# Performance work log

Measured on AMD Instinct MI355X. Metric: run time of the kernel, lower is better.

The kernel has to match this reference:

```python
import jax, jax.numpy as jnp
import numpy as np

B, S, H = 2, 2048, 1024
NH = 16
HD = H // NH  # 64


def setup_inputs() -> dict:
    key = jax.random.key(0)
    ks = jax.random.split(key, 12)
    s = 1.0 / np.sqrt(H)
    return {
        "x_q": jax.random.normal(ks[0], (B, S, H), jnp.float32),
        "x_k": jax.random.normal(ks[1], (B, S, H), jnp.float32),
        "x_v": jax.random.normal(ks[2], (B, S, H), jnp.float32),
        "attention_mask": jax.random.randint(ks[3], (B, S), 0, 2, jnp.int32),
        "Wq": jax.random.normal(ks[4], (H, H), jnp.float32) * s,
        "bq": jnp.zeros((H,), jnp.float32),
        "Wk": jax.random.normal(ks[5], (H, H), jnp.float32) * s,
        "bk": jnp.zeros((H,), jnp.float32),
        "Wv": jax.random.normal(ks[6], (H, H), jnp.float32) * s,
        "bv": jnp.zeros((H,), jnp.float32),
        "Wo": jax.random.normal(ks[7], (H, H), jnp.float32) * s,
        "bo": jnp.zeros((H,), jnp.float32),
    }


def reference(x_q, x_k, x_v, attention_mask, Wq, bq, Wk, bk, Wv, bv, Wo, bo):
    b, s, h = x_q.shape
    # projections
    q = x_q @ Wq + bq
    k = x_k @ Wk + bk
    v = x_v @ Wv + bv
    # [B, NH, S, HD]
    q = q.reshape(b, s, NH, HD).transpose(0, 2, 1, 3)
    k = k.reshape(b, s, NH, HD).transpose(0, 2, 1, 3)
    v = v.reshape(b, s, NH, HD).transpose(0, 2, 1, 3)
    scores = jnp.einsum("bhqd,bhkd->bhqk", q, k) / jnp.sqrt(jnp.float32(HD))
    # key-padding mask: 1 -> keep (0 bias), else -inf; broadcast [B,1,1,S]
    bias = jnp.where(attention_mask == 1, 0.0, -jnp.inf).astype(scores.dtype)
    scores = scores + bias[:, None, None, :]
    attn = jax.nn.softmax(scores, axis=-1)
    # dropout prob = 0.0 (eval / deterministic): identity
    out = jnp.einsum("bhqk,bhkd->bhqd", attn, v)
    out = out.transpose(0, 2, 1, 3).reshape(b, s, h)
    return out @ Wo + bo
```

## Files before the change

kernel.cpp:

```cpp
#include <hip/hip_runtime.h>

#define DEVI static __device__ __forceinline__

typedef unsigned short u16;
typedef unsigned int u32;
typedef __attribute__((ext_vector_type(8))) __bf16 bf16x8;
typedef __attribute__((ext_vector_type(8))) short short8;
typedef __attribute__((ext_vector_type(4))) float f32x4;
typedef __attribute__((ext_vector_type(16))) float f32x16;
typedef __attribute__((ext_vector_type(4))) u32 u32x4;

DEVI u16 f2bf(float f) {
  union { float f; u32 u; } v; v.f = f;
  u32 r = v.u + 0x7fffu + ((v.u >> 16) & 1u);
  return (u16)(r >> 16);
}

DEVI u16 bfc(float f) {
  union { __bf16 b; u16 u; } v; v.b = (__bf16)f; return v.u;
}

DEVI void gload16(const void* g, void* l) {
  __builtin_amdgcn_global_load_lds(
      (const __attribute__((address_space(1))) void*)g,
      (__attribute__((address_space(3))) void*)l,
      16, 0, 0);
}

__global__ void k_cvt(const float* __restrict__ in, u16* __restrict__ out, int n4) {
  int i = blockIdx.x * blockDim.x + threadIdx.x;
  if (i >= n4) return;
  const float4 v = reinterpret_cast<const float4*>(in)[i];
  ushort4 o;
  o.x = f2bf(v.x); o.y = f2bf(v.y); o.z = f2bf(v.z); o.w = f2bf(v.w);
  reinterpret_cast<ushort4*>(out)[i] = o;
}

__global__ void k_maskbias(const int* __restrict__ m, float* __restrict__ bias, int n) {
  int i = blockIdx.x * blockDim.x + threadIdx.x;
  if (i < n) bias[i] = (m[i] == 1) ? 0.f : -1e30f;
}

__global__ void k_transcvt(const float* __restrict__ W, u16* __restrict__ Wt) {
  __shared__ float tl[32][33];
  const int n0 = blockIdx.x * 32, k0 = blockIdx.y * 32;
  const int tx = threadIdx.x, ty = threadIdx.y;
#pragma unroll
  for (int r = ty; r < 32; r += 8)
    tl[r][tx] = W[(size_t)(k0 + r) * 1024 + n0 + tx];
  __syncthreads();
#pragma unroll
  for (int r = ty; r < 32; r += 8)
    Wt[(size_t)(n0 + r) * 1024 + k0 + tx] = f2bf(tl[tx][r]);
}

DEVI void store1(u16* C, size_t i, float v) { C[i] = f2bf(v); }
DEVI void store1(float* C, size_t i, float v) { C[i] = v; }

template <typename OutT>
__global__ __launch_bounds__(256, 2) void k_gemm_bt(
    const u16* __restrict__ Abase, long aZ,
    const u16* __restrict__ Btbase, long bZ,
    const float* __restrict__ bias0, const float* __restrict__ bias1,
    const float* __restrict__ bias2,
    float s0, float s1, float s2,
    OutT* __restrict__ Cbase, long cZ, u16* __restrict__ Vt,
    int M, int N, int K) {
  const int z = blockIdx.z;
  const u16* A  = Abase  + (size_t)z * aZ;
  const u16* Bt = Btbase + (size_t)z * bZ;
  OutT* C = Cbase + (size_t)z * cZ;
  const float* bias = (z == 0) ? bias0 : ((z == 1) ? bias1 : bias2);
  const float scl = (z == 0) ? s0 : ((z == 1) ? s1 : s2);

  __shared__ u16 lsA[128 * 32];
  __shared__ u16 lsB[128 * 32];

  const int t = threadIdx.x;
  const int w = t >> 6, ln = t & 63;
  const int l15 = ln & 15, lhi = ln >> 4;
  const int wr = w >> 1, wc = w & 1;
  const int m0 = blockIdx.x * 128, n0 = blockIdx.y * 128;

  f32x4 acc[4][4] = {};

  for (int kt = 0; kt < K; kt += 32) {
#pragma unroll
    for (int i = 0; i < 2; ++i) {
      const int li = i * 256 + t;
      const int row = li >> 2, cb = (li & 3) << 3;
      gload16(A + (size_t)(m0 + row) * K + kt + cb,
              (char*)lsA + (i * 256 + w * 64) * 16);
      gload16(Bt + (size_t)(n0 + row) * K + kt + cb,
              (char*)lsB + (i * 256 + w * 64) * 16);
    }
    __syncthreads();

    bf16x8 af[4], bf_[4];
#pragma unroll
    for (int m = 0; m < 4; ++m)
      af[m] = *reinterpret_cast<const bf16x8*>(
          &lsA[(wr * 64 + m * 16 + l15) * 32 + lhi * 8]);
#pragma unroll
    for (int n = 0; n < 4; ++n)
      bf_[n] = *reinterpret_cast<const bf16x8*>(
          &lsB[(wc * 64 + n * 16 + l15) * 32 + lhi * 8]);
#pragma unroll
    for (int m = 0; m < 4; ++m)
#pragma unroll
      for (int n = 0; n < 4; ++n)
        acc[m][n] = __builtin_amdgcn_mfma_f32_16x16x32_bf16(af[m], bf_[n], acc[m][n], 0, 0, 0);
    __syncthreads();
  }

  if (Vt != nullptr && z == 2) {
#pragma unroll
    for (int n = 0; n < 4; ++n) {
      const int c = n0 + wc * 64 + n * 16 + l15;
      const float bv = bias[c];
#pragma unroll
      for (int m = 0; m < 4; ++m) {
        const int r = m0 + wr * 64 + m * 16 + lhi * 4;
        ushort4 s4;
#pragma unroll
        for (int j = 0; j < 4; ++j) ((u16*)&s4)[j] = f2bf(acc[m][n][j] + bv);
        *reinterpret_cast<ushort4*>(
            &Vt[((size_t)((r >> 11) * 1024 + c)) * 2048 + (r & 2047)]) = s4;
      }
    }
    return;
  }

#pragma unroll
  for (int n = 0; n < 4; ++n) {
    const int c = n0 + wc * 64 + n * 16 + l15;
    const float bv = bias[c];
#pragma unroll
    for (int m = 0; m < 4; ++m)
#pragma unroll
      for (int j = 0; j < 4; ++j) {
        const int r = m0 + wr * 64 + m * 16 + lhi * 4 + j;
        store1(C, (size_t)r * N + c, (acc[m][n][j] + bv) * scl);
      }
  }
}

__global__ __launch_bounds__(256, 2) void k_attn(
    const u16* __restrict__ Q, const u16* __restrict__ K, const u16* __restrict__ Vt,
    const float* __restrict__ MB, u16* __restrict__ O) {
  __shared__ u16 lsK[2][64][72];
  __shared__ u16 lsV[2][64][72];

  const int t = threadIdx.x, w = t >> 6, ln = t & 63;
  const int l31 = ln & 31, h = ln >> 5, h8 = h * 8;
  const int fid = blockIdx.x;
  const int xcd = fid & 7, slot = fid >> 3;
  const int pair = xcd * 4 + (slot >> 4);
  const int qt = slot & 15;
  const int hh = pair & 15, b = pair >> 4;

  const size_t rowQ = (size_t)b * 2048 + qt * 128 + w * 32;
  const int hc = hh * 64;

  const int srow = t >> 3, scol = (t & 7) << 3;
  const u16* Kg = K + ((size_t)b * 2048 + srow) * 1024 + hc + scol;
  const int half = t & 1;
  const int g16 = ((t & 7) >> 1) << 4;
  const u16* VgA = Vt + ((size_t)(b * 1024 + hc) + srow) * 2048 + g16 + 4 * half;
  const float* MBb = MB + b * 2048;

  bf16x8 qb[4];
#pragma unroll
  for (int ks = 0; ks < 4; ++ks)
    qb[ks] = *reinterpret_cast<const bf16x8*>(
        &Q[(rowQ + l31) * 1024 + hc + ks * 16 + h8]);

  f32x16 o[2] = {};
  float mrow = -1e30f, lsum = 0.f;

  short8 rk0, rk1;
  ushort4 rv0a, rv0b, rv1a, rv1b;
  rk0 = *reinterpret_cast<const short8*>(Kg);
  rk1 = *reinterpret_cast<const short8*>(Kg + 32 * 1024);
  rv0a = *reinterpret_cast<const ushort4*>(VgA);
  rv0b = *reinterpret_cast<const ushort4*>(VgA + 8);
  rv1a = *reinterpret_cast<const ushort4*>(VgA + 32 * 2048);
  rv1b = *reinterpret_cast<const ushort4*>(VgA + 32 * 2048 + 8);
  *reinterpret_cast<short8*>(&lsK[0][srow][scol]) = rk0;
  *reinterpret_cast<short8*>(&lsK[0][32 + srow][scol]) = rk1;
  *reinterpret_cast<ushort4*>(&lsV[0][srow][scol]) = rv0a;
  *reinterpret_cast<ushort4*>(&lsV[0][srow][scol + 4]) = rv0b;
  *reinterpret_cast<ushort4*>(&lsV[0][32 + srow][scol]) = rv1a;
  *reinterpret_cast<ushort4*>(&lsV[0][32 + srow][scol + 4]) = rv1b;
  __syncthreads();

  int cur = 0;
  for (int nt = 0; nt < 2048; nt += 64) {
    const int ntn = (nt + 64 < 2048) ? nt + 64 : 0;
    rk0 = *reinterpret_cast<const short8*>(Kg + (size_t)ntn * 1024);
    rk1 = *reinterpret_cast<const short8*>(Kg + (size_t)(ntn + 32) * 1024);
    rv0a = *reinterpret_cast<const ushort4*>(VgA + ntn);
    rv0b = *reinterpret_cast<const ushort4*>(VgA + ntn + 8);
    rv1a = *reinterpret_cast<const ushort4*>(VgA + 32 * 2048 + ntn);
    rv1b = *reinterpret_cast<const ushort4*>(VgA + 32 * 2048 + ntn + 8);

    f32x16 st[2] = {};
    __builtin_amdgcn_s_setprio(1);
#pragma unroll
    for (int kf2 = 0; kf2 < 2; ++kf2)
#pragma unroll
      for (int ks = 0; ks < 4; ++ks) {
        const bf16x8 kb = *reinterpret_cast<const bf16x8*>(
            &lsK[cur][kf2 * 32 + l31][ks * 16 + h8]);
        st[kf2] = __builtin_amdgcn_mfma_f32_32x32x16_bf16(kb, qb[ks], st[kf2], 0, 0, 0);
      }
    __builtin_amdgcn_s_setprio(0);

#pragma unroll
    for (int f = 0; f < 2; ++f)
#pragma unroll
      for (int rg = 0; rg < 4; ++rg) {
        const f32x4 bv = *reinterpret_cast<const f32x4*>(
            &MBb[nt + f * 32 + rg * 8 + h * 4]);
#pragma unroll
        for (int jj = 0; jj < 4; ++jj) st[f][rg * 4 + jj] += bv[jj];
      }

    float tm = st[0][0];
#pragma unroll
    for (int f = 0; f < 2; ++f)
#pragma unroll
      for (int i = 0; i < 16; ++i) tm = fmaxf(tm, st[f][i]);
    tm = fmaxf(tm, __shfl_xor(tm, 32, 64));

    const bool trig = tm > mrow + 8.f;
    if (__any(trig)) {
      const float al = trig ? __builtin_amdgcn_exp2f(mrow - tm) : 1.f;
      if (trig) mrow = tm;
      lsum *= al;
#pragma unroll
      for (int f = 0; f < 2; ++f)
#pragma unroll
        for (int i = 0; i < 16; ++i) o[f][i] *= al;
    }

    float rs = 0.f;
#pragma unroll
    for (int f = 0; f < 2; ++f)
#pragma unroll
      for (int i = 0; i < 16; ++i) {
        const float p = __builtin_amdgcn_exp2f(st[f][i] - mrow);
        st[f][i] = p;
        rs += p;
      }
    rs += __shfl_xor(rs, 32, 64);
    lsum += rs;

    __builtin_amdgcn_s_setprio(1);
#pragma unroll
    for (int f = 0; f < 2; ++f) {
      u32 pk[8];
#pragma unroll
      for (int i = 0; i < 8; ++i) {
        const u32 lo = bfc(st[f][2 * i]), hi = bfc(st[f][2 * i + 1]);
        pk[i] = lo | (hi << 16);
      }
#pragma unroll
      for (int s = 0; s < 2; ++s) {
        u32x4 pw;
        pw[0] = pk[4 * s + 0]; pw[1] = pk[4 * s + 1];
        pw[2] = pk[4 * s + 2]; pw[3] = pk[4 * s + 3];
        const bf16x8 pb = __builtin_bit_cast(bf16x8, pw);
        const int ks = f * 2 + s;
#pragma unroll
        for (int df2 = 0; df2 < 2; ++df2) {
          const bf16x8 vt = *reinterpret_cast<const bf16x8*>(
              &lsV[cur][df2 * 32 + l31][ks * 16 + h8]);
          o[df2] = __builtin_amdgcn_mfma_f32_32x32x16_bf16(vt, pb, o[df2], 0, 0, 0);
        }
      }
    }
    __builtin_amdgcn_s_setprio(0);

    *reinterpret_cast<short8*>(&lsK[cur ^ 1][srow][scol]) = rk0;
    *reinterpret_cast<short8*>(&lsK[cur ^ 1][32 + srow][scol]) = rk1;
    *reinterpret_cast<ushort4*>(&lsV[cur ^ 1][srow][scol]) = rv0a;
    *reinterpret_cast<ushort4*>(&lsV[cur ^ 1][srow][scol + 4]) = rv0b;
    *reinterpret_cast<ushort4*>(&lsV[cur ^ 1][32 + srow][scol]) = rv1a;
    *reinterpret_cast<ushort4*>(&lsV[cur ^ 1][32 + srow][scol + 4]) = rv1b;
    __syncthreads();
    cur ^= 1;
  }

  const float inv = 1.f / lsum;
#pragma unroll
  for (int df2 = 0; df2 < 2; ++df2)
#pragma unroll
    for (int rg = 0; rg < 4; ++rg) {
      ushort4 s4;
      s4.x = bfc(o[df2][rg * 4 + 0] * inv);
      s4.y = bfc(o[df2][rg * 4 + 1] * inv);
      s4.z = bfc(o[df2][rg * 4 + 2] * inv);
      s4.w = bfc(o[df2][rg * 4 + 3] * inv);
      *reinterpret_cast<ushort4*>(
          &O[(rowQ + l31) * 1024 + hc + df2 * 32 + rg * 8 + h * 4]) = s4;
    }
}

extern "C" void kernel_launch(void* const* d_in, const int* in_sizes, int n_in,
                              void* d_out, int out_size, void* d_ws, size_t ws_size,
                              hipStream_t stream) {
  const float* x_q = (const float*)d_in[0];
  const float* x_k = (const float*)d_in[1];
  const float* x_v = (const float*)d_in[2];
  const int*   msk = (const int*)d_in[3];
  const float* Wq  = (const float*)d_in[4];
  const float* bq  = (const float*)d_in[5];
  const float* Wk  = (const float*)d_in[6];
  const float* bk  = (const float*)d_in[7];
  const float* Wv  = (const float*)d_in[8];
  const float* bv  = (const float*)d_in[9];
  const float* Wo  = (const float*)d_in[10];
  const float* bo  = (const float*)d_in[11];

  const size_t NTOK = 4096, H = 1024;
  u16* xbf  = (u16*)d_ws;
  u16* wt   = xbf + 3 * NTOK * H;
  u16* qkv  = wt  + 4 * H * H;
  u16* aout = qkv + 3 * NTOK * H;
  float* mb = (float*)(aout + NTOK * H);
  u16* vtb  = qkv + 2 * NTOK * H;

  k_cvt<<<dim3(4096), dim3(256), 0, stream>>>(x_q, xbf,              1048576);
  k_cvt<<<dim3(4096), dim3(256), 0, stream>>>(x_k, xbf + NTOK * H,   1048576);
  k_cvt<<<dim3(4096), dim3(256), 0, stream>>>(x_v, xbf + 2 * NTOK * H, 1048576);
  k_maskbias<<<dim3(16), dim3(256), 0, stream>>>(msk, mb, 4096);
  k_transcvt<<<dim3(32, 32), dim3(32, 8), 0, stream>>>(Wq, wt);
  k_transcvt<<<dim3(32, 32), dim3(32, 8), 0, stream>>>(Wk, wt + H * H);
  k_transcvt<<<dim3(32, 32), dim3(32, 8), 0, stream>>>(Wv, wt + 2 * H * H);
  k_transcvt<<<dim3(32, 32), dim3(32, 8), 0, stream>>>(Wo, wt + 3 * H * H);

  const float qscale = 0.125f * 1.4426950408889634f;
  k_gemm_bt<u16><<<dim3(32, 8, 3), dim3(256), 0, stream>>>(
      xbf, (long)(NTOK * H), wt, (long)(H * H), bq, bk, bv,
      qscale, 1.f, 1.f,
      qkv, (long)(NTOK * H), vtb, 4096, 1024, 1024);

  k_attn<<<dim3(512), dim3(256), 0, stream>>>(
      qkv, qkv + NTOK * H, vtb, mb, aout);

  k_gemm_bt<float><<<dim3(32, 8, 1), dim3(256), 0, stream>>>(
      aout, 0L, wt + 3 * H * H, 0L, bo, bo, bo,
      1.f, 1.f, 1.f,
      (float*)d_out, 0L, nullptr, 4096, 1024, 1024);
}
```

Baseline: 159.5 us.

## Software-pipeline attention QK^T one tile ahead and batch conversion launches

Restructures the attention loop so the QK^T MFMAs for the next key tile are issued before the softmax and PV of the current tile. K gets a triple-buffered LDS ring and V stays double-buffered, with global prefetch two or three tiles ahead and the loop manually unrolled by two to alternate score registers. Separately, the three input-conversion launches and four weight-transpose launches are merged into single launches using grid z/y. This adds LDS and register pressure, which could reduce occupancy under the 2-block launch bound.

Result: faster. 149.2 us (-6.5%).

```diff
diff --git a/kernel.cpp b/kernel.cpp
--- a/kernel.cpp
+++ b/kernel.cpp
@@ -27,13 +27,17 @@
       16, 0, 0);
 }
 
-__global__ void k_cvt(const float* __restrict__ in, u16* __restrict__ out, int n4) {
-  int i = blockIdx.x * blockDim.x + threadIdx.x;
+__global__ void k_cvt3(const float* __restrict__ a, const float* __restrict__ b2,
+                       const float* __restrict__ c, u16* __restrict__ out, int n4) {
+  const int z = blockIdx.y;
+  const float* in = (z == 0) ? a : ((z == 1) ? b2 : c);
+  u16* o = out + (size_t)z * (size_t)n4 * 4;
+  const int i = blockIdx.x * blockDim.x + threadIdx.x;
   if (i >= n4) return;
   const float4 v = reinterpret_cast<const float4*>(in)[i];
-  ushort4 o;
-  o.x = f2bf(v.x); o.y = f2bf(v.y); o.z = f2bf(v.z); o.w = f2bf(v.w);
-  reinterpret_cast<ushort4*>(out)[i] = o;
+  ushort4 s;
+  s.x = f2bf(v.x); s.y = f2bf(v.y); s.z = f2bf(v.z); s.w = f2bf(v.w);
+  reinterpret_cast<ushort4*>(o)[i] = s;
 }
 
 __global__ void k_maskbias(const int* __restrict__ m, float* __restrict__ bias, int n) {
@@ -41,7 +45,12 @@
   if (i < n) bias[i] = (m[i] == 1) ? 0.f : -1e30f;
 }
 
-__global__ void k_transcvt(const float* __restrict__ W, u16* __restrict__ Wt) {
+__global__ void k_transcvt4(const float* __restrict__ W0, const float* __restrict__ W1,
+                            const float* __restrict__ W2, const float* __restrict__ W3,
+                            u16* __restrict__ Wtb) {
+  const int z = blockIdx.z;
+  const float* W = (z == 0) ? W0 : ((z == 1) ? W1 : ((z == 2) ? W2 : W3));
+  u16* Wt = Wtb + (size_t)z * 1024 * 1024;
   __shared__ float tl[32][33];
   const int n0 = blockIdx.x * 32, k0 = blockIdx.y * 32;
   const int tx = threadIdx.x, ty = threadIdx.y;
@@ -148,7 +157,7 @@
 __global__ __launch_bounds__(256, 2) void k_attn(
     const u16* __restrict__ Q, const u16* __restrict__ K, const u16* __restrict__ Vt,
     const float* __restrict__ MB, u16* __restrict__ O) {
-  __shared__ u16 lsK[2][64][72];
+  __shared__ u16 lsK[3][64][72];
   __shared__ u16 lsV[2][64][72];
 
   const int t = threadIdx.x, w = t >> 6, ln = t & 63;
@@ -175,122 +184,139 @@
     qb[ks] = *reinterpret_cast<const bf16x8*>(
         &Q[(rowQ + l31) * 1024 + hc + ks * 16 + h8]);
 
-  f32x16 o[2] = {};
+  f32x16 o[2];
+#pragma unroll
+  for (int i = 0; i < 16; ++i) { o[0][i] = 0.f; o[1][i] = 0.f; }
   float mrow = -1e30f, lsum = 0.f;
 
-  short8 rk0, rk1;
-  ushort4 rv0a, rv0b, rv1a, rv1b;
-  rk0 = *reinterpret_cast<const short8*>(Kg);
-  rk1 = *reinterpret_cast<const short8*>(Kg + 32 * 1024);
-  rv0a = *reinterpret_cast<const ushort4*>(VgA);
-  rv0b = *reinterpret_cast<const ushort4*>(VgA + 8);
-  rv1a = *reinterpret_cast<const ushort4*>(VgA + 32 * 2048);
-  rv1b = *reinterpret_cast<const ushort4*>(VgA + 32 * 2048 + 8);
-  *reinterpret_cast<short8*>(&lsK[0][srow][scol]) = rk0;
-  *reinterpret_cast<short8*>(&lsK[0][32 + srow][scol]) = rk1;
-  *reinterpret_cast<ushort4*>(&lsV[0][srow][scol]) = rv0a;
-  *reinterpret_cast<ushort4*>(&lsV[0][srow][scol + 4]) = rv0b;
-  *reinterpret_cast<ushort4*>(&lsV[0][32 + srow][scol]) = rv1a;
-  *reinterpret_cast<ushort4*>(&lsV[0][32 + srow][scol + 4]) = rv1b;
+#pragma unroll
+  for (int p = 0; p < 3; ++p) {
+    const short8 a = *reinterpret_cast<const short8*>(Kg + (size_t)(p * 64) * 1024);
+    const short8 c = *reinterpret_cast<const short8*>(Kg + (size_t)(p * 64 + 32) * 1024);
+    *reinterpret_cast<short8*>(&lsK[p][srow][scol]) = a;
+    *reinterpret_cast<short8*>(&lsK[p][32 + srow][scol]) = c;
+  }
+#pragma unroll
+  for (int p = 0; p < 2; ++p) {
+    const ushort4 a = *reinterpret_cast<const ushort4*>(VgA + p * 64);
+    const ushort4 b4 = *reinterpret_cast<const ushort4*>(VgA + p * 64 + 8);
+    const ushort4 c = *reinterpret_cast<const ushort4*>(VgA + 32 * 2048 + p * 64);
+    const ushort4 d = *reinterpret_cast<const ushort4*>(VgA + 32 * 2048 + p * 64 + 8);
+    *reinterpret_cast<ushort4*>(&lsV[p][srow][scol]) = a;
+    *reinterpret_cast<ushort4*>(&lsV[p][srow][scol + 4]) = b4;
+    *reinterpret_cast<ushort4*>(&lsV[p][32 + srow][scol]) = c;
+    *reinterpret_cast<ushort4*>(&lsV[p][32 + srow][scol + 4]) = d;
+  }
   __syncthreads();
 
-  int cur = 0;
-  for (int nt = 0; nt < 2048; nt += 64) {
-    const int ntn = (nt + 64 < 2048) ? nt + 64 : 0;
-    rk0 = *reinterpret_cast<const short8*>(Kg + (size_t)ntn * 1024);
-    rk1 = *reinterpret_cast<const short8*>(Kg + (size_t)(ntn + 32) * 1024);
-    rv0a = *reinterpret_cast<const ushort4*>(VgA + ntn);
-    rv0b = *reinterpret_cast<const ushort4*>(VgA + ntn + 8);
-    rv1a = *reinterpret_cast<const ushort4*>(VgA + 32 * 2048 + ntn);
-    rv1b = *reinterpret_cast<const ushort4*>(VgA + 32 * 2048 + ntn + 8);
-
-    f32x16 st[2] = {};
-    __builtin_amdgcn_s_setprio(1);
-#pragma unroll
-    for (int kf2 = 0; kf2 < 2; ++kf2)
-#pragma unroll
-      for (int ks = 0; ks < 4; ++ks) {
-        const bf16x8 kb = *reinterpret_cast<const bf16x8*>(
-            &lsK[cur][kf2 * 32 + l31][ks * 16 + h8]);
-        st[kf2] = __builtin_amdgcn_mfma_f32_32x32x16_bf16(kb, qb[ks], st[kf2], 0, 0, 0);
-      }
-    __builtin_amdgcn_s_setprio(0);
-
-#pragma unroll
-    for (int f = 0; f < 2; ++f)
-#pragma unroll
-      for (int rg = 0; rg < 4; ++rg) {
-        const f32x4 bv = *reinterpret_cast<const f32x4*>(
-            &MBb[nt + f * 32 + rg * 8 + h * 4]);
-#pragma unroll
-        for (int jj = 0; jj < 4; ++jj) st[f][rg * 4 + jj] += bv[jj];
-      }
-
-    float tm = st[0][0];
-#pragma unroll
-    for (int f = 0; f < 2; ++f)
-#pragma unroll
-      for (int i = 0; i < 16; ++i) tm = fmaxf(tm, st[f][i]);
-    tm = fmaxf(tm, __shfl_xor(tm, 32, 64));
-
-    const bool trig = tm > mrow + 8.f;
-    if (__any(trig)) {
-      const float al = trig ? __builtin_amdgcn_exp2f(mrow - tm) : 1.f;
-      if (trig) mrow = tm;
-      lsum *= al;
-#pragma unroll
-      for (int f = 0; f < 2; ++f)
-#pragma unroll
-        for (int i = 0; i < 16; ++i) o[f][i] *= al;
-    }
-
-    float rs = 0.f;
-#pragma unroll
-    for (int f = 0; f < 2; ++f)
-#pragma unroll
-      for (int i = 0; i < 16; ++i) {
-        const float p = __builtin_amdgcn_exp2f(st[f][i] - mrow);
-        st[f][i] = p;
-        rs += p;
-      }
-    rs += __shfl_xor(rs, 32, 64);
-    lsum += rs;
-
-    __builtin_amdgcn_s_setprio(1);
-#pragma unroll
-    for (int f = 0; f < 2; ++f) {
-      u32 pk[8];
-#pragma unroll
-      for (int i = 0; i < 8; ++i) {
-        const u32 lo = bfc(st[f][2 * i]), hi = bfc(st[f][2 * i + 1]);
-        pk[i] = lo | (hi << 16);
-      }
-#pragma unroll
-      for (int s = 0; s < 2; ++s) {
-        u32x4 pw;
-        pw[0] = pk[4 * s + 0]; pw[1] = pk[4 * s + 1];
-        pw[2] = pk[4 * s + 2]; pw[3] = pk[4 * s + 3];
-        const bf16x8 pb = __builtin_bit_cast(bf16x8, pw);
-        const int ks = f * 2 + s;
-#pragma unroll
-        for (int df2 = 0; df2 < 2; ++df2) {
-          const bf16x8 vt = *reinterpret_cast<const bf16x8*>(
-              &lsV[cur][df2 * 32 + l31][ks * 16 + h8]);
-          o[df2] = __builtin_amdgcn_mfma_f32_32x32x16_bf16(vt, pb, o[df2], 0, 0, 0);
-        }
-      }
-    }
-    __builtin_amdgcn_s_setprio(0);
-
-    *reinterpret_cast<short8*>(&lsK[cur ^ 1][srow][scol]) = rk0;
-    *reinterpret_cast<short8*>(&lsK[cur ^ 1][32 + srow][scol]) = rk1;
-    *reinterpret_cast<ushort4*>(&lsV[cur ^ 1][srow][scol]) = rv0a;
-    *reinterpret_cast<ushort4*>(&lsV[cur ^ 1][srow][scol + 4]) = rv0b;
-    *reinterpret_cast<ushort4*>(&lsV[cur ^ 1][32 + srow][scol]) = rv1a;
-    *reinterpret_cast<ushort4*>(&lsV[cur ^ 1][32 + srow][scol + 4]) = rv1b;
-    __syncthreads();
-    cur ^= 1;
-  }
+  f32x16 stA[2], stB[2];
+#pragma unroll
+  for (int i = 0; i < 16; ++i) { stA[0][i] = 0.f; stA[1][i] = 0.f; }
+#pragma unroll
+  for (int ks = 0; ks < 4; ++ks) {
+    const bf16x8 kb0 = *reinterpret_cast<const bf16x8*>(&lsK[0][l31][ks * 16 + h8]);
+    const bf16x8 kb1 = *reinterpret_cast<const bf16x8*>(&lsK[0][32 + l31][ks * 16 + h8]);
+    stA[0] = __builtin_amdgcn_mfma_f32_32x32x16_bf16(kb0, qb[ks], stA[0], 0, 0, 0);
+    stA[1] = __builtin_amdgcn_mfma_f32_32x32x16_bf16(kb1, qb[ks], stA[1], 0, 0, 0);
+  }
+
+#define ATTN_BODY(T, CUR, NXT, SW)                                                  \
+  {                                                                                 \
+    const int tK = ((T) + 3) & 31, tV = ((T) + 2) & 31;                             \
+    const short8 rk0 = *reinterpret_cast<const short8*>(Kg + (size_t)(tK * 64) * 1024); \
+    const short8 rk1 = *reinterpret_cast<const short8*>(Kg + (size_t)(tK * 64 + 32) * 1024); \
+    const ushort4 rv0a = *reinterpret_cast<const ushort4*>(VgA + tV * 64);          \
+    const ushort4 rv0b = *reinterpret_cast<const ushort4*>(VgA + tV * 64 + 8);      \
+    const ushort4 rv1a = *reinterpret_cast<const ushort4*>(VgA + 32 * 2048 + tV * 64); \
+    const ushort4 rv1b = *reinterpret_cast<const ushort4*>(VgA + 32 * 2048 + tV * 64 + 8); \
+    const int sK = ((SW) == 2) ? 0 : (SW) + 1;                                      \
+    _Pragma("unroll")                                                               \
+    for (int i = 0; i < 16; ++i) { NXT[0][i] = 0.f; NXT[1][i] = 0.f; }              \
+    __builtin_amdgcn_s_setprio(1);                                                  \
+    _Pragma("unroll")                                                               \
+    for (int ks = 0; ks < 4; ++ks) {                                                \
+      const bf16x8 kb0 = *reinterpret_cast<const bf16x8*>(&lsK[sK][l31][ks * 16 + h8]); \
+      const bf16x8 kb1 = *reinterpret_cast<const bf16x8*>(&lsK[sK][32 + l31][ks * 16 + h8]); \
+      NXT[0] = __builtin_amdgcn_mfma_f32_32x32x16_bf16(kb0, qb[ks], NXT[0], 0, 0, 0); \
+      NXT[1] = __builtin_amdgcn_mfma_f32_32x32x16_bf16(kb1, qb[ks], NXT[1], 0, 0, 0); \
+    }                                                                               \
+    __builtin_amdgcn_s_setprio(0);                                                  \
+    _Pragma("unroll")                                                               \
+    for (int f = 0; f < 2; ++f)                                                     \
+      _Pragma("unroll")                                                             \
+      for (int rg = 0; rg < 4; ++rg) {                                              \
+        const f32x4 bv = *reinterpret_cast<const f32x4*>(                           \
+            &MBb[(T) * 64 + f * 32 + rg * 8 + h * 4]);                              \
+        _Pragma("unroll")                                                           \
+        for (int jj = 0; jj < 4; ++jj) CUR[f][rg * 4 + jj] += bv[jj];               \
+      }                                                                             \
+    float tm = CUR[0][0];                                                           \
+    _Pragma("unroll")                                                               \
+    for (int f = 0; f < 2; ++f)                                                     \
+      _Pragma("unroll")                                                             \
+      for (int i = 0; i < 16; ++i) tm = fmaxf(tm, CUR[f][i]);                       \
+    tm = fmaxf(tm, __shfl_xor(tm, 32, 64));                                         \
+    const bool trig = tm > mrow + 8.f;                                              \
+    if (__any(trig)) {                                                              \
+      const float al = trig ? __builtin_amdgcn_exp2f(mrow - tm) : 1.f;              \
+      if (trig) mrow = tm;                                                          \
+      lsum *= al;                                                                   \
+      _Pragma("unroll")                                                             \
+      for (int f = 0; f < 2; ++f)                                                   \
+        _Pragma("unroll")                                                           \
+        for (int i = 0; i < 16; ++i) o[f][i] *= al;                                 \
+    }                                                                               \
+    float rs = 0.f;                                                                 \
+    _Pragma("unroll")                                                               \
+    for (int f = 0; f < 2; ++f)                                                     \
+      _Pragma("unroll")                                                             \
+      for (int i = 0; i < 16; ++i) {                                                \
+        const float p = __builtin_amdgcn_exp2f(CUR[f][i] - mrow);                   \
+        CUR[f][i] = p;                                                              \
+        rs += p;                                                                    \
+      }                                                                             \
+    rs += __shfl_xor(rs, 32, 64);                                                   \
+    lsum += rs;                                                                     \
+    __builtin_amdgcn_s_setprio(1);                                                  \
+    _Pragma("unroll")                                                               \
+    for (int f = 0; f < 2; ++f) {                                                   \
+      u32 pk[8];                                                                    \
+      _Pragma("unroll")                                                             \
+      for (int i = 0; i < 8; ++i)                                                   \
+        pk[i] = (u32)bfc(CUR[f][2 * i]) | ((u32)bfc(CUR[f][2 * i + 1]) << 16);      \
+      _Pragma("unroll")                                                             \
+      for (int s = 0; s < 2; ++s) {                                                 \
+        u32x4 pw;                                                                   \
+        pw[0] = pk[4 * s + 0]; pw[1] = pk[4 * s + 1];                               \
+        pw[2] = pk[4 * s + 2]; pw[3] = pk[4 * s + 3];                               \
+        const bf16x8 pb = __builtin_bit_cast(bf16x8, pw);                           \
+        const int ks = f * 2 + s;                                                   \
+        _Pragma("unroll")                                                           \
+        for (int df2 = 0; df2 < 2; ++df2) {                                         \
+          const bf16x8 vt = *reinterpret_cast<const bf16x8*>(                       \
+              &lsV[(T) & 1][df2 * 32 + l31][ks * 16 + h8]);                         \
+          o[df2] = __builtin_amdgcn_mfma_f32_32x32x16_bf16(vt, pb, o[df2], 0, 0, 0); \
+        }                                                                           \
+      }                                                                             \
+    }                                                                               \
+    __builtin_amdgcn_s_setprio(0);                                                  \
+    __syncthreads();                                                                \
+    *reinterpret_cast<short8*>(&lsK[SW][srow][scol]) = rk0;                         \
+    *reinterpret_cast<short8*>(&lsK[SW][32 + srow][scol]) = rk1;                    \
+    *reinterpret_cast<ushort4*>(&lsV[(T) & 1][srow][scol]) = rv0a;                  \
+    *reinterpret_cast<ushort4*>(&lsV[(T) & 1][srow][scol + 4]) = rv0b;              \
+    *reinterpret_cast<ushort4*>(&lsV[(T) & 1][32 + srow][scol]) = rv1a;             \
+    *reinterpret_cast<ushort4*>(&lsV[(T) & 1][32 + srow][scol + 4]) = rv1b;         \
+  }
+
+  int sw = 0;
+  for (int t2 = 0; t2 < 32; t2 += 2) {
+    ATTN_BODY(t2, stA, stB, sw);
+    sw = (sw == 2) ? 0 : sw + 1;
+    ATTN_BODY(t2 + 1, stB, stA, sw);
+    sw = (sw == 2) ? 0 : sw + 1;
+  }
+#undef ATTN_BODY
 
   const float inv = 1.f / lsum;
 #pragma unroll
@@ -331,14 +357,9 @@
   float* mb = (float*)(aout + NTOK * H);
   u16* vtb  = qkv + 2 * NTOK * H;
 
-  k_cvt<<<dim3(4096), dim3(256), 0, stream>>>(x_q, xbf,              1048576);
-  k_cvt<<<dim3(4096), dim3(256), 0, stream>>>(x_k, xbf + NTOK * H,   1048576);
-  k_cvt<<<dim3(4096), dim3(256), 0, stream>>>(x_v, xbf + 2 * NTOK * H, 1048576);
+  k_cvt3<<<dim3(4096, 3), dim3(256), 0, stream>>>(x_q, x_k, x_v, xbf, 1048576);
   k_maskbias<<<dim3(16), dim3(256), 0, stream>>>(msk, mb, 4096);
-  k_transcvt<<<dim3(32, 32), dim3(32, 8), 0, stream>>>(Wq, wt);
-  k_transcvt<<<dim3(32, 32), dim3(32, 8), 0, stream>>>(Wk, wt + H * H);
-  k_transcvt<<<dim3(32, 32), dim3(32, 8), 0, stream>>>(Wv, wt + 2 * H * H);
-  k_transcvt<<<dim3(32, 32), dim3(32, 8), 0, stream>>>(Wo, wt + 3 * H * H);
+  k_transcvt4<<<dim3(32, 32, 4), dim3(32, 8), 0, stream>>>(Wq, Wk, Wv, Wo, wt);
 
   const float qscale = 0.125f * 1.4426950408889634f;
   k_gemm_bt<u16><<<dim3(32, 8, 3), dim3(256), 0, stream>>>(
```
